# Optimization experiments

Hardware: AMD Instinct MI355X
Metric: run time of the kernel (lower is better)

Reference implementation:

```python
import jax, jax.numpy as jnp
import numpy as np

N_NODES = 10000
N_EDGES = 640000
D_IN, D_HID, D_OUT = 128, 256, 64


def setup_inputs() -> dict:
    key = jax.random.key(0)
    k = jax.random.split(key, 8)
    h = jax.random.normal(k[0], (N_NODES, D_IN), dtype=jnp.float32)
    w = jax.random.uniform(k[1], (N_EDGES, 1), dtype=jnp.float32)
    src = jax.random.randint(k[2], (N_EDGES,), 0, N_NODES, dtype=jnp.int32)
    dst = jax.random.randint(k[3], (N_EDGES,), 0, N_NODES, dtype=jnp.int32)
    W1 = jax.random.normal(k[4], (2 * D_IN, D_HID), dtype=jnp.float32) * (1.0 / np.sqrt(2 * D_IN))
    b1 = jnp.zeros((D_HID,), dtype=jnp.float32)
    W2 = jax.random.normal(k[5], (2 * D_HID, D_OUT), dtype=jnp.float32) * (1.0 / np.sqrt(2 * D_HID))
    b2 = jnp.zeros((D_OUT,), dtype=jnp.float32)
    return {"h": h, "w": w, "src": src, "dst": dst, "W1": W1, "b1": b1, "W2": W2, "b2": b2}


def _sage_layer(h, w, src, dst, W, b, n_nodes):
    # message: m_e = h[src_e] * w_e  (scalar edge weight broadcast over features)
    m = h[src] * w  # [E, D]
    # mean scatter-reduce over incoming edges per destination node
    s = jax.ops.segment_sum(m, dst, num_segments=n_nodes)          # [N, D]
    deg = jax.ops.segment_sum(jnp.ones((dst.shape[0],), h.dtype), dst, num_segments=n_nodes)
    h_N = jnp.where(deg[:, None] > 0, s / jnp.maximum(deg, 1.0)[:, None], 0.0)
    # concat + linear
    return jnp.concatenate([h, h_N], axis=1) @ W + b


def reference(h, w, src, dst, W1, b1, W2, b2):
    n = h.shape[0]
    x = _sage_layer(h, w, src, dst, W1, b1, n)
    x = jax.nn.relu(x)
    return _sage_layer(x, w, src, dst, W2, b2, n)
```

## Files before the change

kernel.cpp:

```cpp
#include <hip/hip_runtime.h>
#include <hip/hip_fp16.h>


#define NSUB 4
#define CAPS 64
#define FB 2048

typedef _Float16 f16x8 __attribute__((ext_vector_type(8)));
typedef float f32x4 __attribute__((ext_vector_type(4)));

#define ACC8(q, wt)                                              \
  {                                                              \
    const float2 t0 = __half22float2(*(const __half2*)&(q).x);   \
    const float2 t1 = __half22float2(*(const __half2*)&(q).y);   \
    const float2 t2 = __half22float2(*(const __half2*)&(q).z);   \
    const float2 t3 = __half22float2(*(const __half2*)&(q).w);   \
    a[0] += t0.x * (wt); a[1] += t0.y * (wt);                    \
    a[2] += t1.x * (wt); a[3] += t1.y * (wt);                    \
    a[4] += t2.x * (wt); a[5] += t2.y * (wt);                    \
    a[6] += t3.x * (wt); a[7] += t3.y * (wt);                    \
  }


__global__ __launch_bounds__(256) void fill_k(const int* __restrict__ src,
                                              const int* __restrict__ dst,
                                              const float* __restrict__ w,
                                              const float* __restrict__ h,
                                              const float* __restrict__ W1,
                                              const float* __restrict__ W2,
                                              int* __restrict__ cursor,
                                              unsigned int* __restrict__ ebuf,
                                              __half* __restrict__ hh,
                                              __half* __restrict__ W1z,
                                              __half* __restrict__ W2z,
                                              int E, int N, int NH4) {
  if (blockIdx.x < FB) {
    const int grp = blockIdx.x & 7;
    const int bi = blockIdx.x >> 3;
    const int nbg = FB >> 3;
    const int chunk = (N + 7) >> 3;
    const int lo = grp * chunk;
    const int hi = min(N, lo + chunk);
    for (int i = bi * 256 + threadIdx.x; i < E; i += nbg * 256) {
      const int d = dst[i];
      if (d >= lo && d < hi) {
        const int sub = i & (NSUB - 1);
        const int p = atomicAdd(&cursor[d * NSUB + sub], 1);
        if (p < CAPS) {
          const __half hw = __float2half_rn(w[i]);
          ebuf[((size_t)(d * NSUB + sub)) * CAPS + p] =
              ((unsigned int)src[i] << 16) | (unsigned int)__half_as_ushort(hw);
        }
      }
    }
    return;
  }
  const int t = (blockIdx.x - FB) * 256 + threadIdx.x;
  if (t < NH4) {
    const float4 v = reinterpret_cast<const float4*>(h)[t];
    reinterpret_cast<__half2*>(hh)[2 * t] = __floats2half2_rn(v.x, v.y);
    reinterpret_cast<__half2*>(hh)[2 * t + 1] = __floats2half2_rn(v.z, v.w);
    return;
  }
  const int tw1 = t - NH4;
  if (tw1 < 8192) {
    const int ln = tw1 & 63;
    const int nt = (tw1 >> 6) & 15;
    const int kc = tw1 >> 10;
    const int kbase = kc * 32 + (ln >> 4) * 8;
    const int n = nt * 16 + (ln & 15);
    __half tmp[8];
#pragma unroll
    for (int j = 0; j < 8; ++j)
      tmp[j] = __float2half_rn(W1[(size_t)(kbase + j) * 256 + n]);
    *reinterpret_cast<uint4*>(W1z + (size_t)tw1 * 8) = *reinterpret_cast<uint4*>(tmp);
    return;
  }
  const int tw2 = tw1 - 8192;
  if (tw2 < 4096) {
    const int ln = tw2 & 63;
    const int nt = (tw2 >> 6) & 7;
    const int kc = tw2 >> 9;
    const int kbase = kc * 32 + (ln >> 4) * 8;
    const int np = nt * 16 + (ln & 15);
    __half tmp[8];
#pragma unroll
    for (int j = 0; j < 8; ++j) {
      const int k = kbase + j;
      const float v = (np < 64) ? W2[(size_t)k * 64 + np]
                                : W2[(size_t)(256 + k) * 64 + (np - 64)];
      tmp[j] = __float2half_rn(v);
    }
    *reinterpret_cast<uint4*>(W2z + (size_t)tw2 * 8) = *reinterpret_cast<uint4*>(tmp);
  }
}


__global__ __launch_bounds__(256) void agg1_k(const __half* __restrict__ hh,
                                              const unsigned int* __restrict__ ebuf,
                                              const int* __restrict__ cnt,
                                              __half* __restrict__ G1, int N) {
  const int chunk = (N + 7) >> 3;
  const int g8 = blockIdx.x & 7;
  const int k = blockIdx.x >> 3;
  const int wv = threadIdx.x >> 6;
  const int node_sel = wv >> 1;
  const int half = wv & 1;
  const int loc = k * 2 + node_sel;
  const int n = g8 * chunk + loc;
  const int lane = threadIdx.x & 63;
  const int g = lane >> 4;
  const int f = lane & 15;
  const uint4* __restrict__ H = reinterpret_cast<const uint4*>(hh);
  __shared__ float part[2][2][16][8];
  __shared__ int degs[2][2];
  const bool valid = (loc < chunk) && (n < N);

  int m0 = 0, m1 = 0;
  unsigned int pk0 = 0, pk1 = 0;
  if (valid) {
    const int base = n * NSUB + half * 2;
    const int2 c2 = *reinterpret_cast<const int2*>(cnt + base);
    m0 = min(c2.x, CAPS);
    m1 = min(c2.y, CAPS);
    const unsigned int* __restrict__ bkt0 = ebuf + (size_t)base * CAPS;
    pk0 = (lane < m0) ? bkt0[lane] : 0u;
    pk1 = (lane < m1) ? bkt0[CAPS + lane] : 0u;
  }
  const int deg = m0 + m1;
  const int mMax = max(m0, m1);

  float a[8] = {};
  for (int j = 0; j < mMax; j += 8) {
    const unsigned int pA = __shfl(pk0, j + g);
    const unsigned int pB = __shfl(pk0, j + 4 + g);
    const unsigned int pC = __shfl(pk1, j + g);
    const unsigned int pD = __shfl(pk1, j + 4 + g);
    const uint4 qA = H[(size_t)(pA >> 16) * 16 + f];
    const uint4 qB = H[(size_t)(pB >> 16) * 16 + f];
    const uint4 qC = H[(size_t)(pC >> 16) * 16 + f];
    const uint4 qD = H[(size_t)(pD >> 16) * 16 + f];
    const float wA = __half2float(__ushort_as_half((unsigned short)pA));
    const float wB = __half2float(__ushort_as_half((unsigned short)pB));
    const float wC = __half2float(__ushort_as_half((unsigned short)pC));
    const float wD = __half2float(__ushort_as_half((unsigned short)pD));
    ACC8(qA, wA)
    ACC8(qB, wB)
    ACC8(qC, wC)
    ACC8(qD, wD)
  }
#pragma unroll
  for (int r = 0; r < 8; ++r) {
    a[r] += __shfl_xor(a[r], 16);
    a[r] += __shfl_xor(a[r], 32);
  }
  if (lane < 16) {
#pragma unroll
    for (int r = 0; r < 8; ++r) part[node_sel][half][f][r] = a[r];
    if (f == 0) degs[node_sel][half] = deg;
  }
  __syncthreads();
  if (half == 0 && lane < 16 && valid) {
    const int d = degs[node_sel][0] + degs[node_sel][1];
    const float inv = (d > 0) ? 1.0f / (float)d : 0.0f;
    __half tmp[8];
#pragma unroll
    for (int r = 0; r < 8; ++r)
      tmp[r] = __float2half_rn((part[node_sel][0][f][r] + part[node_sel][1][f][r]) * inv);
    reinterpret_cast<uint4*>(G1)[(size_t)n * 16 + f] = *reinterpret_cast<uint4*>(tmp);
  }
}


__global__ __launch_bounds__(256) void gemm1zu_k(const __half* __restrict__ hh,
                                                 const __half* __restrict__ G1,
                                                 const __half* __restrict__ W1z,
                                                 const float* __restrict__ b1,
                                                 const __half* __restrict__ W2z,
                                                 __half* __restrict__ Z,
                                                 float* __restrict__ U) {
  const int tid = threadIdx.x;
  const int w = tid >> 6, lane = tid & 63;
  const int m0 = blockIdx.x * 16;
  const int row_in = m0 + (lane & 15);
  const int qoff = (lane >> 4) * 8;
  const int colq = lane & 15;
  const int rowq = (lane >> 4) * 4;

  f32x4 acc[4] = {};
  const __half* __restrict__ Ah = hh + (size_t)row_in * 128;
  const __half* __restrict__ Ag = G1 + (size_t)row_in * 128;
#pragma unroll
  for (int kc = 0; kc < 8; ++kc) {
    const __half* asrc = (kc < 4) ? (Ah + kc * 32 + qoff) : (Ag + (kc - 4) * 32 + qoff);
    const f16x8 af = *reinterpret_cast<const f16x8*>(asrc);
    const __half* bbase = W1z + ((size_t)(kc * 16 + w * 4) * 64 + lane) * 8;
#pragma unroll
    for (int nt = 0; nt < 4; ++nt) {
      const f16x8 bf = *reinterpret_cast<const f16x8*>(bbase + (size_t)nt * 64 * 8);
      acc[nt] = __builtin_amdgcn_mfma_f32_16x16x32_f16(af, bf, acc[nt], 0, 0, 0);
    }
  }
  __shared__ alignas(16) __half Hs[16][264];
#pragma unroll
  for (int nt = 0; nt < 4; ++nt) {
    const int col = w * 64 + nt * 16 + colq;
    const float bz = b1[col];
#pragma unroll
    for (int r = 0; r < 4; ++r)
      Hs[rowq + r][col] = __float2half_rn(fmaxf(acc[nt][r] + bz, 0.f));
  }
  __syncthreads();

  f32x4 accz[2] = {};
#pragma unroll
  for (int kc = 0; kc < 8; ++kc) {
    const f16x8 af = *reinterpret_cast<const f16x8*>(&Hs[lane & 15][kc * 32 + qoff]);
    const __half* bbase = W2z + ((size_t)(kc * 8 + w * 2) * 64 + lane) * 8;
#pragma unroll
    for (int nt = 0; nt < 2; ++nt) {
      const f16x8 bf = *reinterpret_cast<const f16x8*>(bbase + (size_t)nt * 64 * 8);
      accz[nt] = __builtin_amdgcn_mfma_f32_16x16x32_f16(af, bf, accz[nt], 0, 0, 0);
    }
  }
  __shared__ float S[16][132];
#pragma unroll
  for (int nt = 0; nt < 2; ++nt) {
    const int col = w * 32 + nt * 16 + colq;
#pragma unroll
    for (int r = 0; r < 4; ++r) S[rowq + r][col] = accz[nt][r];
  }
  __syncthreads();
  {
    const int row = tid >> 4, c4 = tid & 15;
    const float4 v = make_float4(S[row][c4 * 4], S[row][c4 * 4 + 1],
                                 S[row][c4 * 4 + 2], S[row][c4 * 4 + 3]);
    *reinterpret_cast<float4*>(&U[(size_t)(m0 + row) * 64 + c4 * 4]) = v;
  }
  if (tid < 128) {
    const int row = tid >> 3, c8 = tid & 7;
    const float* s = &S[row][64 + c8 * 8];
    const __half2 h0 = __floats2half2_rn(s[0], s[1]);
    const __half2 h1 = __floats2half2_rn(s[2], s[3]);
    const __half2 h2 = __floats2half2_rn(s[4], s[5]);
    const __half2 h3 = __floats2half2_rn(s[6], s[7]);
    uint4 q;
    q.x = *reinterpret_cast<const unsigned int*>(&h0);
    q.y = *reinterpret_cast<const unsigned int*>(&h1);
    q.z = *reinterpret_cast<const unsigned int*>(&h2);
    q.w = *reinterpret_cast<const unsigned int*>(&h3);
    *reinterpret_cast<uint4*>(&Z[(size_t)(m0 + row) * 64 + c8 * 8]) = q;
  }
}


__global__ __launch_bounds__(256) void agg2z_k(const __half* __restrict__ Z,
                                               const float* __restrict__ U,
                                               const float* __restrict__ b2,
                                               const unsigned int* __restrict__ ebuf,
                                               const int* __restrict__ cnt,
                                               float* __restrict__ out, int N) {
  const int chunk = (N + 7) >> 3;
  const int g8 = blockIdx.x & 7;
  const int k = blockIdx.x >> 3;
  const int loc = k * 4 + (threadIdx.x >> 6);
  const int n = g8 * chunk + loc;
  if (loc >= chunk || n >= N) return;
  const int lane = threadIdx.x & 63;
  const int g = lane >> 3;
  const int f = lane & 7;
  const uint4* __restrict__ Zr = reinterpret_cast<const uint4*>(Z);

  const int4 c4 = *reinterpret_cast<const int4*>(cnt + n * NSUB);
  int m[NSUB];
  m[0] = min(c4.x, CAPS);
  m[1] = min(c4.y, CAPS);
  m[2] = min(c4.z, CAPS);
  m[3] = min(c4.w, CAPS);
  const int deg = m[0] + m[1] + m[2] + m[3];
  const int mMax = max(max(m[0], m[1]), max(m[2], m[3]));

  const unsigned int* __restrict__ bkt = ebuf + ((size_t)(n * NSUB)) * CAPS;
  unsigned int pk[NSUB];
#pragma unroll
  for (int s = 0; s < NSUB; ++s)
    pk[s] = (lane < m[s]) ? bkt[s * CAPS + lane] : 0u;

  float a[8] = {};
  for (int j = 0; j < mMax; j += 16) {
    unsigned int pA[NSUB], pB[NSUB];
#pragma unroll
    for (int s = 0; s < NSUB; ++s) {
      pA[s] = __shfl(pk[s], j + g);
      pB[s] = __shfl(pk[s], j + 8 + g);
    }
    uint4 qA[NSUB], qB[NSUB];
#pragma unroll
    for (int s = 0; s < NSUB; ++s) {
      qA[s] = Zr[(size_t)(pA[s] >> 16) * 8 + f];
      qB[s] = Zr[(size_t)(pB[s] >> 16) * 8 + f];
    }
#pragma unroll
    for (int s = 0; s < NSUB; ++s) {
      const float wA = __half2float(__ushort_as_half((unsigned short)pA[s]));
      const float wB = __half2float(__ushort_as_half((unsigned short)pB[s]));
      ACC8(qA[s], wA)
      ACC8(qB[s], wB)
    }
  }
#pragma unroll
  for (int r = 0; r < 8; ++r) {
    a[r] += __shfl_xor(a[r], 8);
    a[r] += __shfl_xor(a[r], 16);
    a[r] += __shfl_xor(a[r], 32);
  }
  if (lane < 8) {
    const float inv = (deg > 0) ? 1.0f / (float)deg : 0.0f;
    const float4 u0 = *reinterpret_cast<const float4*>(&U[(size_t)n * 64 + f * 8]);
    const float4 u1 = *reinterpret_cast<const float4*>(&U[(size_t)n * 64 + f * 8 + 4]);
    const float4 z0 = *reinterpret_cast<const float4*>(&b2[f * 8]);
    const float4 z1 = *reinterpret_cast<const float4*>(&b2[f * 8 + 4]);
    float4 o0, o1;
    o0.x = a[0] * inv + u0.x + z0.x;
    o0.y = a[1] * inv + u0.y + z0.y;
    o0.z = a[2] * inv + u0.z + z0.z;
    o0.w = a[3] * inv + u0.w + z0.w;
    o1.x = a[4] * inv + u1.x + z1.x;
    o1.y = a[5] * inv + u1.y + z1.y;
    o1.z = a[6] * inv + u1.z + z1.z;
    o1.w = a[7] * inv + u1.w + z1.w;
    *reinterpret_cast<float4*>(&out[(size_t)n * 64 + f * 8]) = o0;
    *reinterpret_cast<float4*>(&out[(size_t)n * 64 + f * 8 + 4]) = o1;
  }
}


extern "C" void kernel_launch(void* const* d_in, const int* in_sizes, int n_in,
                              void* d_out, int out_size, void* d_ws, size_t ws_size,
                              hipStream_t stream) {
  const float* h   = (const float*)d_in[0];
  const float* w   = (const float*)d_in[1];
  const int*   src = (const int*)d_in[2];
  const int*   dst = (const int*)d_in[3];
  const float* W1  = (const float*)d_in[4];
  const float* b1  = (const float*)d_in[5];
  const float* W2  = (const float*)d_in[6];
  const float* b2  = (const float*)d_in[7];
  float* out = (float*)d_out;

  const int N = in_sizes[0] / 128;
  const int E = in_sizes[2];

  char* ws = (char*)d_ws;
  size_t o = 0;
  auto alloc = [&](size_t bytes) -> void* {
    void* p = ws + o;
    o = (o + bytes + 255) & ~(size_t)255;
    return p;
  };
  int*          cursor = (int*)alloc((size_t)N * NSUB * 4);
  unsigned int* ebuf   = (unsigned int*)alloc((size_t)N * NSUB * CAPS * 4);
  __half*       hh     = (__half*)alloc((size_t)N * 128 * 2);
  __half*       G1     = (__half*)alloc((size_t)N * 128 * 2);
  __half*       Z      = (__half*)alloc((size_t)N * 64 * 2);
  float*        U      = (float*)alloc((size_t)N * 64 * 4);
  __half*       W1z    = (__half*)alloc((size_t)256 * 256 * 2);
  __half*       W2z    = (__half*)alloc((size_t)256 * 128 * 2);

  const int NH4 = N * 32;
  const int prep_blocks = (NH4 + 8192 + 4096 + 255) / 256;
  const int chunk = (N + 7) >> 3;

  hipMemsetAsync(cursor, 0, (size_t)N * NSUB * 4, stream);
  fill_k<<<FB + prep_blocks, 256, 0, stream>>>(src, dst, w, h, W1, W2, cursor,
                                               ebuf, hh, W1z, W2z, E, N, NH4);
  agg1_k<<<8 * ((chunk + 1) / 2), 256, 0, stream>>>(hh, ebuf, cursor, G1, N);
  gemm1zu_k<<<N / 16, 256, 0, stream>>>(hh, G1, W1z, b1, W2z, Z, U);
  agg2z_k<<<8 * ((chunk + 3) / 4), 256, 0, stream>>>(Z, U, b2, ebuf, cursor, out, N);
}
```

Baseline: 137.6 us.

## Fuse layer-1 neighbor aggregation into the MFMA GEMM kernel via shared memory

Result: no change. 137.9 us (+0.2%).

```diff
diff --git a/kernel.cpp b/kernel.cpp
--- a/kernel.cpp
+++ b/kernel.cpp
@@ -96,103 +96,94 @@
 }
 
 
-__global__ __launch_bounds__(256) void agg1_k(const __half* __restrict__ hh,
+__global__ __launch_bounds__(256) void ag1g_k(const __half* __restrict__ hh,
                                               const unsigned int* __restrict__ ebuf,
                                               const int* __restrict__ cnt,
-                                              __half* __restrict__ G1, int N) {
+                                              const __half* __restrict__ W1z,
+                                              const float* __restrict__ b1,
+                                              const __half* __restrict__ W2z,
+                                              __half* __restrict__ Z,
+                                              float* __restrict__ U, int N) {
   const int chunk = (N + 7) >> 3;
   const int g8 = blockIdx.x & 7;
-  const int k = blockIdx.x >> 3;
-  const int wv = threadIdx.x >> 6;
-  const int node_sel = wv >> 1;
-  const int half = wv & 1;
-  const int loc = k * 2 + node_sel;
-  const int n = g8 * chunk + loc;
-  const int lane = threadIdx.x & 63;
+  const int kb = blockIdx.x >> 3;
+  const int locbase = kb * 16;
+  const int nbase = g8 * chunk + locbase;
+  const int tid = threadIdx.x;
+  const int wv = tid >> 6;
+  const int lane = tid & 63;
   const int g = lane >> 4;
   const int f = lane & 15;
+
+  __shared__ alignas(16) __half As[16][136];
+  __shared__ alignas(16) __half Hs[16][264];
+  __shared__ alignas(16) float S[16][132];
+
   const uint4* __restrict__ H = reinterpret_cast<const uint4*>(hh);
-  __shared__ float part[2][2][16][8];
-  __shared__ int degs[2][2];
-  const bool valid = (loc < chunk) && (n < N);
-
-  int m0 = 0, m1 = 0;
-  unsigned int pk0 = 0, pk1 = 0;
-  if (valid) {
-    const int base = n * NSUB + half * 2;
-    const int2 c2 = *reinterpret_cast<const int2*>(cnt + base);
-    m0 = min(c2.x, CAPS);
-    m1 = min(c2.y, CAPS);
-    const unsigned int* __restrict__ bkt0 = ebuf + (size_t)base * CAPS;
-    pk0 = (lane < m0) ? bkt0[lane] : 0u;
-    pk1 = (lane < m1) ? bkt0[CAPS + lane] : 0u;
-  }
-  const int deg = m0 + m1;
-  const int mMax = max(m0, m1);
-
-  float a[8] = {};
-  for (int j = 0; j < mMax; j += 8) {
-    const unsigned int pA = __shfl(pk0, j + g);
-    const unsigned int pB = __shfl(pk0, j + 4 + g);
-    const unsigned int pC = __shfl(pk1, j + g);
-    const unsigned int pD = __shfl(pk1, j + 4 + g);
-    const uint4 qA = H[(size_t)(pA >> 16) * 16 + f];
-    const uint4 qB = H[(size_t)(pB >> 16) * 16 + f];
-    const uint4 qC = H[(size_t)(pC >> 16) * 16 + f];
-    const uint4 qD = H[(size_t)(pD >> 16) * 16 + f];
-    const float wA = __half2float(__ushort_as_half((unsigned short)pA));
-    const float wB = __half2float(__ushort_as_half((unsigned short)pB));
-    const float wC = __half2float(__ushort_as_half((unsigned short)pC));
-    const float wD = __half2float(__ushort_as_half((unsigned short)pD));
-    ACC8(qA, wA)
-    ACC8(qB, wB)
-    ACC8(qC, wC)
-    ACC8(qD, wD)
-  }
-#pragma unroll
-  for (int r = 0; r < 8; ++r) {
-    a[r] += __shfl_xor(a[r], 16);
-    a[r] += __shfl_xor(a[r], 32);
-  }
-  if (lane < 16) {
-#pragma unroll
-    for (int r = 0; r < 8; ++r) part[node_sel][half][f][r] = a[r];
-    if (f == 0) degs[node_sel][half] = deg;
+
+#pragma unroll
+  for (int i = 0; i < 4; ++i) {
+    const int row = wv * 4 + i;
+    const int loc = locbase + row;
+    const int n = g8 * chunk + loc;
+    const bool valid = (loc < chunk) && (n < N);
+    int m[NSUB] = {0, 0, 0, 0};
+    unsigned int pk[NSUB] = {0u, 0u, 0u, 0u};
+    if (valid) {
+      const int4 c4 = *reinterpret_cast<const int4*>(cnt + n * NSUB);
+      m[0] = min(c4.x, CAPS);
+      m[1] = min(c4.y, CAPS);
+      m[2] = min(c4.z, CAPS);
+      m[3] = min(c4.w, CAPS);
+      const unsigned int* __restrict__ bkt = ebuf + ((size_t)(n * NSUB)) * CAPS;
+#pragma unroll
+      for (int s = 0; s < NSUB; ++s)
+        pk[s] = (lane < m[s]) ? bkt[s * CAPS + lane] : 0u;
+    }
+    const int deg = m[0] + m[1] + m[2] + m[3];
+    const int mMax = max(max(m[0], m[1]), max(m[2], m[3]));
+
+    float a[8] = {};
+    for (int j = 0; j < mMax; j += 4) {
+      unsigned int p[NSUB];
+#pragma unroll
+      for (int s = 0; s < NSUB; ++s) p[s] = __shfl(pk[s], j + g);
+      uint4 q[NSUB];
+#pragma unroll
+      for (int s = 0; s < NSUB; ++s) q[s] = H[(size_t)(p[s] >> 16) * 16 + f];
+#pragma unroll
+      for (int s = 0; s < NSUB; ++s) {
+        const float wt = __half2float(__ushort_as_half((unsigned short)p[s]));
+        ACC8(q[s], wt)
+      }
+    }
+#pragma unroll
+    for (int r = 0; r < 8; ++r) {
+      a[r] += __shfl_xor(a[r], 16);
+      a[r] += __shfl_xor(a[r], 32);
+    }
+    if (lane < 16) {
+      const float inv = (deg > 0) ? 1.0f / (float)deg : 0.0f;
+      __half tmp[8];
+#pragma unroll
+      for (int r = 0; r < 8; ++r) tmp[r] = __float2half_rn(a[r] * inv);
+      *reinterpret_cast<uint4*>(&As[row][f * 8]) = *reinterpret_cast<uint4*>(tmp);
+    }
   }
   __syncthreads();
-  if (half == 0 && lane < 16 && valid) {
-    const int d = degs[node_sel][0] + degs[node_sel][1];
-    const float inv = (d > 0) ? 1.0f / (float)d : 0.0f;
-    __half tmp[8];
-#pragma unroll
-    for (int r = 0; r < 8; ++r)
-      tmp[r] = __float2half_rn((part[node_sel][0][f][r] + part[node_sel][1][f][r]) * inv);
-    reinterpret_cast<uint4*>(G1)[(size_t)n * 16 + f] = *reinterpret_cast<uint4*>(tmp);
-  }
-}
-
-
-__global__ __launch_bounds__(256) void gemm1zu_k(const __half* __restrict__ hh,
-                                                 const __half* __restrict__ G1,
-                                                 const __half* __restrict__ W1z,
-                                                 const float* __restrict__ b1,
-                                                 const __half* __restrict__ W2z,
-                                                 __half* __restrict__ Z,
-                                                 float* __restrict__ U) {
-  const int tid = threadIdx.x;
-  const int w = tid >> 6, lane = tid & 63;
-  const int m0 = blockIdx.x * 16;
-  const int row_in = m0 + (lane & 15);
+
+  const int w = wv;
+  const int row_in = nbase + (lane & 15);
   const int qoff = (lane >> 4) * 8;
   const int colq = lane & 15;
   const int rowq = (lane >> 4) * 4;
 
   f32x4 acc[4] = {};
   const __half* __restrict__ Ah = hh + (size_t)row_in * 128;
-  const __half* __restrict__ Ag = G1 + (size_t)row_in * 128;
 #pragma unroll
   for (int kc = 0; kc < 8; ++kc) {
-    const __half* asrc = (kc < 4) ? (Ah + kc * 32 + qoff) : (Ag + (kc - 4) * 32 + qoff);
+    const __half* asrc =
+        (kc < 4) ? (Ah + kc * 32 + qoff) : (&As[lane & 15][(kc - 4) * 32 + qoff]);
     const f16x8 af = *reinterpret_cast<const f16x8*>(asrc);
     const __half* bbase = W1z + ((size_t)(kc * 16 + w * 4) * 64 + lane) * 8;
 #pragma unroll
@@ -201,7 +192,6 @@
       acc[nt] = __builtin_amdgcn_mfma_f32_16x16x32_f16(af, bf, acc[nt], 0, 0, 0);
     }
   }
-  __shared__ alignas(16) __half Hs[16][264];
 #pragma unroll
   for (int nt = 0; nt < 4; ++nt) {
     const int col = w * 64 + nt * 16 + colq;
@@ -223,7 +213,6 @@
       accz[nt] = __builtin_amdgcn_mfma_f32_16x16x32_f16(af, bf, accz[nt], 0, 0, 0);
     }
   }
-  __shared__ float S[16][132];
 #pragma unroll
   for (int nt = 0; nt < 2; ++nt) {
     const int col = w * 32 + nt * 16 + colq;
@@ -233,23 +222,27 @@
   __syncthreads();
   {
     const int row = tid >> 4, c4 = tid & 15;
-    const float4 v = make_float4(S[row][c4 * 4], S[row][c4 * 4 + 1],
-                                 S[row][c4 * 4 + 2], S[row][c4 * 4 + 3]);
-    *reinterpret_cast<float4*>(&U[(size_t)(m0 + row) * 64 + c4 * 4]) = v;
+    if (locbase + row < chunk && nbase + row < N) {
+      const float4 v = make_float4(S[row][c4 * 4], S[row][c4 * 4 + 1],
+                                   S[row][c4 * 4 + 2], S[row][c4 * 4 + 3]);
+      *reinterpret_cast<float4*>(&U[(size_t)(nbase + row) * 64 + c4 * 4]) = v;
+    }
   }
   if (tid < 128) {
     const int row = tid >> 3, c8 = tid & 7;
-    const float* s = &S[row][64 + c8 * 8];
-    const __half2 h0 = __floats2half2_rn(s[0], s[1]);
-    const __half2 h1 = __floats2half2_rn(s[2], s[3]);
-    const __half2 h2 = __floats2half2_rn(s[4], s[5]);
-    const __half2 h3 = __floats2half2_rn(s[6], s[7]);
-    uint4 q;
-    q.x = *reinterpret_cast<const unsigned int*>(&h0);
-    q.y = *reinterpret_cast<const unsigned int*>(&h1);
-    q.z = *reinterpret_cast<const unsigned int*>(&h2);
-    q.w = *reinterpret_cast<const unsigned int*>(&h3);
-    *reinterpret_cast<uint4*>(&Z[(size_t)(m0 + row) * 64 + c8 * 8]) = q;
+    if (locbase + row < chunk && nbase + row < N) {
+      const float* s = &S[row][64 + c8 * 8];
+      const __half2 h0 = __floats2half2_rn(s[0], s[1]);
+      const __half2 h1 = __floats2half2_rn(s[2], s[3]);
+      const __half2 h2 = __floats2half2_rn(s[4], s[5]);
+      const __half2 h3 = __floats2half2_rn(s[6], s[7]);
+      uint4 q;
+      q.x = *reinterpret_cast<const unsigned int*>(&h0);
+      q.y = *reinterpret_cast<const unsigned int*>(&h1);
+      q.z = *reinterpret_cast<const unsigned int*>(&h2);
+      q.w = *reinterpret_cast<const unsigned int*>(&h3);
+      *reinterpret_cast<uint4*>(&Z[(size_t)(nbase + row) * 64 + c8 * 8]) = q;
+    }
   }
 }
 
@@ -361,7 +354,6 @@
   int*          cursor = (int*)alloc((size_t)N * NSUB * 4);
   unsigned int* ebuf   = (unsigned int*)alloc((size_t)N * NSUB * CAPS * 4);
   __half*       hh     = (__half*)alloc((size_t)N * 128 * 2);
-  __half*       G1     = (__half*)alloc((size_t)N * 128 * 2);
   __half*       Z      = (__half*)alloc((size_t)N * 64 * 2);
   float*        U      = (float*)alloc((size_t)N * 64 * 4);
   __half*       W1z    = (__half*)alloc((size_t)256 * 256 * 2);
@@ -374,7 +366,7 @@
   hipMemsetAsync(cursor, 0, (size_t)N * NSUB * 4, stream);
   fill_k<<<FB + prep_blocks, 256, 0, stream>>>(src, dst, w, h, W1, W2, cursor,
                                                ebuf, hh, W1z, W2z, E, N, NH4);
-  agg1_k<<<8 * ((chunk + 1) / 2), 256, 0, stream>>>(hh, ebuf, cursor, G1, N);
-  gemm1zu_k<<<N / 16, 256, 0, stream>>>(hh, G1, W1z, b1, W2z, Z, U);
+  ag1g_k<<<8 * ((chunk + 15) >> 4), 256, 0, stream>>>(hh, ebuf, cursor, W1z, b1,
+                                                      W2z, Z, U, N);
   agg2z_k<<<8 * ((chunk + 3) / 4), 256, 0, stream>>>(Z, U, b2, ebuf, cursor, out, N);
 }
```
